# Kernel tuning notes

Hardware: AMD Instinct MI355X
Metric: run time of the kernel (lower is better)

Reference implementation:

```python
import jax, jax.numpy as jnp
import numpy as np

B, L, E = 64, 256, 512
H = 1024          # hidden_size
N = 128           # memory_size
HS = 64           # head_size (memory width)
NH = 4            # NTM heads
OUT = 1024        # output_size
TNH = 4           # transformer nhead
IN_DIM = E + NH * HS          # 768
POD = H + NH * HS             # 1280


def ln(x, g, b, eps=1e-5):
    mu = x.mean(-1, keepdims=True)
    v = ((x - mu) ** 2).mean(-1, keepdims=True)
    return (x - mu) / jnp.sqrt(v + eps) * g + b


def setup_inputs() -> dict:
    key = jax.random.key(0)
    ks = iter(jax.random.split(key, 64))
    def w(shape, s=0.05):
        return jax.random.normal(next(ks), shape, jnp.float32) * s
    f32 = jnp.float32
    return dict(
        x_emb=jax.random.normal(next(ks), (B, L, E), f32),
        in_g=jnp.ones(IN_DIM, f32), in_b=jnp.zeros(IN_DIM, f32),
        W_ih=w((4 * H, IN_DIM)), W_hh=w((4 * H, H)),
        b_ih=jnp.zeros(4 * H, f32), b_hh=jnp.zeros(4 * H, f32),
        cn_g=jnp.ones(H, f32), cn_b=jnp.zeros(H, f32),
        W_rk=w((NH * HS, H)), b_rk=jnp.zeros(NH * HS, f32),
        W_wk=w((NH * HS, H)), b_wk=jnp.zeros(NH * HS, f32),
        W_ws=w((NH, H)), b_ws=jnp.zeros(NH, f32),
        W_ev=w((NH * HS, H)), b_ev=jnp.zeros(NH * HS, f32),
        attn_w=w((3 * HS, HS)), attn_b=jnp.zeros(3 * HS, f32),
        attn_ow=w((HS, HS)), attn_ob=jnp.zeros(HS, f32),
        l1_w=w((2 * HS, HS)), l1_b=jnp.zeros(2 * HS, f32),
        l2_w=w((HS, 2 * HS)), l2_b=jnp.zeros(HS, f32),
        tn1_g=jnp.ones(HS, f32), tn1_b=jnp.zeros(HS, f32),
        tn2_g=jnp.ones(HS, f32), tn2_b=jnp.zeros(HS, f32),
        rkn_g=jnp.ones(HS, f32), rkn_b=jnp.zeros(HS, f32),
        wkn_g=jnp.ones(HS, f32), wkn_b=jnp.zeros(HS, f32),
        mn_g=jnp.ones(HS, f32), mn_b=jnp.zeros(HS, f32),
        po_g=jnp.ones(POD, f32), po_b=jnp.zeros(POD, f32),
        W_proj=w((OUT, POD)), b_proj=jnp.zeros(OUT, f32),
    )


def reference(x_emb, in_g, in_b, W_ih, W_hh, b_ih, b_hh, cn_g, cn_b,
              W_rk, b_rk, W_wk, b_wk, W_ws, b_ws, W_ev, b_ev,
              attn_w, attn_b, attn_ow, attn_ob, l1_w, l1_b, l2_w, l2_b,
              tn1_g, tn1_b, tn2_g, tn2_b, rkn_g, rkn_b, wkn_g, wkn_b,
              mn_g, mn_b, po_g, po_b, W_proj, b_proj):
    Bc = x_emb.shape[0]
    dh = HS // TNH

    def tblock(mem):  # [B, N, HS], eval-mode (dropout = identity)
        qkv = mem @ attn_w.T + attn_b
        q, k, v = jnp.split(qkv, 3, axis=-1)
        q = q.reshape(Bc, N, TNH, dh)
        k = k.reshape(Bc, N, TNH, dh)
        v = v.reshape(Bc, N, TNH, dh)
        a = jax.nn.softmax(jnp.einsum('bqhd,bkhd->bhqk', q, k) / jnp.sqrt(jnp.float32(dh)), axis=-1)
        o = jnp.einsum('bhqk,bkhd->bqhd', a, v).reshape(Bc, N, HS)
        o = o @ attn_ow.T + attn_ob
        x = ln(mem + o, tn1_g, tn1_b)
        ff = jax.nn.gelu(x @ l1_w.T + l1_b, approximate=False) @ l2_w.T + l2_b
        return ln(x + ff, tn2_g, tn2_b)

    def step(carry, x_t):
        h, c, mem, rc = carry
        inp = ln(jnp.concatenate([x_t, rc.reshape(Bc, -1)], axis=-1), in_g, in_b)
        gates = inp @ W_ih.T + b_ih + h @ W_hh.T + b_hh  # torch gate order i,f,g,o
        i, f, g, o = jnp.split(gates, 4, axis=-1)
        c = jax.nn.sigmoid(f) * c + jax.nn.sigmoid(i) * jnp.tanh(g)
        h = jax.nn.sigmoid(o) * jnp.tanh(c)
        hn = ln(h, cn_g, cn_b)
        rk = (hn @ W_rk.T + b_rk).reshape(Bc, NH, HS)
        wk = (hn @ W_wk.T + b_wk).reshape(Bc, NH, HS)
        ws = jax.nn.sigmoid(hn @ W_ws.T + b_ws)                    # [B, NH]
        ev = jax.nn.sigmoid(hn @ W_ev.T + b_ev).reshape(Bc, NH, HS)
        # addressing
        mem = tblock(mem)
        mem_n = ln(mem, mn_g, mn_b)
        rk = ln(rk, rkn_g, rkn_b)
        wk = ln(wk, wkn_g, wkn_b)
        rw = jax.nn.softmax(jnp.einsum('bnk,bmk->bnm', rk, mem_n), axis=-1)
        rc = jnp.einsum('bnm,bmh->bnh', rw, mem)
        ww = jax.nn.softmax(jnp.einsum('bnk,bmk->bnm', wk, mem_n), axis=-1)
        erase = jnp.einsum('bnm,bnh->bmh', ww, ev)
        mem = mem * (1.0 - erase)
        add = jnp.einsum('bnm,bnh->bmh', ww, ws[..., None] * wk)
        mem = mem + add
        out = ln(jnp.concatenate([hn, rc.reshape(Bc, -1)], axis=-1), po_g, po_b)
        logits = out @ W_proj.T + b_proj
        return (h, c, mem, rc), logits

    h0 = jnp.zeros((Bc, H), x_emb.dtype)
    c0 = jnp.zeros((Bc, H), x_emb.dtype)
    mem0 = jnp.zeros((Bc, N, HS), x_emb.dtype)
    rc0 = jnp.zeros((Bc, NH, HS), x_emb.dtype)
    (h, c, mem, _), outs = jax.lax.scan(step, (h0, c0, mem0, rc0), jnp.swapaxes(x_emb, 0, 1))
    return jnp.swapaxes(outs, 0, 1), mem, (h[None], c[None])
```

## Files before the change

kernel.cpp:

```cpp
#include <hip/hip_runtime.h>
#include <math.h>

typedef short s8v __attribute__((ext_vector_type(8)));
typedef float f32x4 __attribute__((ext_vector_type(4)));

__device__ inline float sigm(float x) { return 1.0f / (1.0f + expf(-x)); }
__device__ inline float dot4(const float4 a, const float4 b) {
  return a.x*b.x + a.y*b.y + a.z*b.z + a.w*b.w;
}
__device__ inline float wsum(float v) {
#pragma unroll
  for (int o = 32; o > 0; o >>= 1) v += __shfl_xor(v, o, 64);
  return v;
}
__device__ inline short f2bf(float f) {
  unsigned int u = __float_as_uint(f);
  unsigned int r = u + 0x7FFFu + ((u >> 16) & 1u);
  return (short)(r >> 16);
}
__device__ inline float bf2f(short h) {
  return __uint_as_float(((unsigned int)(unsigned short)h) << 16);
}
__device__ inline void storesplit(float v, short* __restrict__ hi,
                                  short* __restrict__ lo, size_t idx) {
// ... 58 lines not shown
{
  __shared__ float rs[4], rq[4];
  int b = blockIdx.x, tid = threadIdx.x, lane = tid & 63, wid = tid >> 6;
  float v3[3]; float s = 0.f, sq = 0.f;
#pragma unroll
  for (int i = 0; i < 3; i++) {
    int k = tid + i * 256;
    float v = (k < 512) ? x_emb[(size_t)b * 256 * 512 + k] : 0.f;
    v3[i] = v; s += v; sq += v * v;
  }
  s = wsum(s); sq = wsum(sq);
  if (lane == 0) { rs[wid] = s; rq[wid] = sq; }
  __syncthreads();
  float ts = rs[0]+rs[1]+rs[2]+rs[3], tq = rq[0]+rq[1]+rq[2]+rq[3];
  float mu = ts / 768.f, var = tq / 768.f - mu * mu;
  float rstd = rsqrtf(var + 1e-5f);
#pragma unroll
  for (int i = 0; i < 3; i++) {
    int k = tid + i * 256;
    storesplit((v3[i] - mu) * rstd * in_g[k] + in_b[k], inbH, inbL, b*1792 + k);
  }
}

__global__ __launch_bounds__(256) void kA(
    const short* __restrict__ inbH, const short* __restrict__ inbL,
    short* __restrict__ inbHn, short* __restrict__ inbLn,
    const short* __restrict__ WgH, const short* __restrict__ WgL,
    const float* __restrict__ b_ih, const float* __restrict__ b_hh,
    float* __restrict__ cbuf, float* __restrict__ hbuf,
    float* __restrict__ hstat, float* __restrict__ gatesP,
    unsigned* __restrict__ tick,
    const short* __restrict__ membH, const short* __restrict__ membL,
    const short* __restrict__ WqH, const short* __restrict__ WqL,
    const float* __restrict__ attn_b,
    const short* __restrict__ pob16, const short* __restrict__ Wp16,
    const float* __restrict__ b_proj,
    float* __restrict__ qkv, float* __restrict__ outs, int t)
{
  __shared__ char poolA[40960];
  __shared__ unsigned sOld;
  int bid = blockIdx.x, tid = threadIdx.x, lane = tid & 63, w = tid >> 6;
  if (bid < 128) {
    if (t >= 256) return;
    short (*sT)[4][2560] = (short(*)[4][2560])poolA;
    int jt = bid & 63, kt = bid >> 6;
    int k0 = kt * 896;
    int srow = tid >> 2, scol = (tid & 3) * 8;
    const short* gAH = inbH + srow*1792 + k0 + scol;
    const short* gAL = inbL + srow*1792 + k0 + scol;
    const short* gBH = WgH + (size_t)(jt*64 + srow)*1792 + k0 + scol;
    const short* gBL = WgL + (size_t)(jt*64 + srow)*1792 + k0 + scol;
    int4 rAH = *(const int4*)gAH, rAL = *(const int4*)gAL;
    int4 rBH = *(const int4*)gBH, rBL = *(const int4*)gBL;
    *(int4*)&sT[0][0][srow*40 + scol] = rAH;
    *(int4*)&sT[0][1][srow*40 + scol] = rAL;
    *(int4*)&sT[0][2][srow*40 + scol] = rBH;
    *(int4*)&sT[0][3][srow*40 + scol] = rBL;
    f32x4 acc[4] = {};
    int arow = lane & 15, akk = (lane >> 4) * 8;
    for (int c = 0; c < 28; ++c) {
      int cur = c & 1;
      if (c < 27) {
        rAH = *(const int4*)(gAH + (c+1)*32);
        rAL = *(const int4*)(gAL + (c+1)*32);
        rBH = *(const int4*)(gBH + (c+1)*32);
        rBL = *(const int4*)(gBL + (c+1)*32);
      }
      __syncthreads();
      s8v bh = *(const s8v*)&sT[cur][2][(w*16 + arow)*40 + akk];
      s8v bl = *(const s8v*)&sT[cur][3][(w*16 + arow)*40 + akk];
#pragma unroll
      for (int ms = 0; ms < 4; ++ms) {
        s8v ah = *(const s8v*)&sT[cur][0][(arow + ms*16)*40 + akk];
        s8v al = *(const s8v*)&sT[cur][1][(arow + ms*16)*40 + akk];
        acc[ms] = __builtin_amdgcn_mfma_f32_16x16x32_bf16(ah, bh, acc[ms], 0,0,0);
        acc[ms] = __builtin_amdgcn_mfma_f32_16x16x32_bf16(al, bh, acc[ms], 0,0,0);
        acc[ms] = __builtin_amdgcn_mfma_f32_16x16x32_bf16(ah, bl, acc[ms], 0,0,0);
      }
      if (c < 27) {
        *(int4*)&sT[cur^1][0][srow*40 + scol] = rAH;
        *(int4*)&sT[cur^1][1][srow*40 + scol] = rAL;
        *(int4*)&sT[cur^1][2][srow*40 + scol] = rBH;
        *(int4*)&sT[cur^1][3][srow*40 + scol] = rBL;
      }
    }
    {
      float* gp = gatesP + (size_t)kt * 262144;
      int j = jt*64 + w*16 + (lane & 15);
#pragma unroll
      for (int ms = 0; ms < 4; ms++)
#pragma unroll
        for (int r = 0; r < 4; r++) {
          int b = ms*16 + (lane>>4)*4 + r;
          gp[b*4096 + j] = acc[ms][r];
        }
    }
    __syncthreads();
    if (tid == 0) {
      __threadfence();
      sOld = __hip_atomic_fetch_add(&tick[jt], 1u, __ATOMIC_ACQ_REL,
                                    __HIP_MEMORY_SCOPE_AGENT);
    }
    __syncthreads();
    if (!(sOld & 1u)) return;
    {
      const float* pp = gatesP + (size_t)(kt^1) * 262144;
      int j = jt*64 + w*16 + (lane & 15);
#pragma unroll
      for (int ms = 0; ms < 4; ms++)
#pragma unroll
        for (int r = 0; r < 4; r++) {
          int b = ms*16 + (lane>>4)*4 + r;
          acc[ms][r] += __hip_atomic_load(&pp[b*4096 + j], __ATOMIC_RELAXED,
                                          __HIP_MEMORY_SCOPE_AGENT);
        }
    }
    float* sC = (float*)poolA;
    float* sRed = (float*)(poolA + 17408);
    __syncthreads();
    {
      int rr = w*16 + (lane & 15);
#pragma unroll
      for (int ms = 0; ms < 4; ms++)
#pragma unroll
        for (int r = 0; r < 4; r++) {
          int b = ms*16 + (lane>>4)*4 + r;
          sC[b*68 + rr] = acc[ms][r];
        }
    }
    __syncthreads();
    {
      int b = tid & 63;
      float sh = 0.f, sh2 = 0.f;
#pragma unroll
      for (int q = 0; q < 4; q++) {
        int ul = (tid >> 6) + q*4;
        int u = jt*16 + ul;
        float gi_ = sC[b*68 + ul*4 + 0] + b_ih[u]        + b_hh[u];
        float gf  = sC[b*68 + ul*4 + 1] + b_ih[1024 + u] + b_hh[1024 + u];
        float gg  = sC[b*68 + ul*4 + 2] + b_ih[2048 + u] + b_hh[2048 + u];
        float go  = sC[b*68 + ul*4 + 3] + b_ih[3072 + u] + b_hh[3072 + u];
        float cn = sigm(gf)*cbuf[b*1024 + u] + sigm(gi_)*tanhf(gg);
        float hh = sigm(go)*tanhf(cn);
        cbuf[b*1024 + u] = cn;
        hbuf[b*1024 + u] = hh;
        storesplit(hh, inbHn, inbLn, b*1792 + 768 + u);
        sh += hh; sh2 += hh*hh;
      }
      sRed[(tid>>6)*64 + b] = sh;
      sRed[256 + (tid>>6)*64 + b] = sh2;
    }
    __syncthreads();
    if (tid < 64) {
      float s0 = sRed[tid]+sRed[64+tid]+sRed[128+tid]+sRed[192+tid];
      float s1 = sRed[256+tid]+sRed[320+tid]+sRed[384+tid]+sRed[448+tid];
      hstat[(tid*64 + jt)*2]     = s0;
      hstat[(tid*64 + jt)*2 + 1] = s1;
    }
  } else if (bid < 192) {
    if (t >= 256) return;
    int b = bid - 128;
    const short* Ah = membH + (size_t)b * 8192;
    const short* Al = membL + (size_t)b * 8192;
    int ao = (w*32 + (lane & 15)) * 64 + (lane >> 4) * 8;
    s8v ah00 = *(const s8v*)(Ah + ao);
    s8v ah01 = *(const s8v*)(Ah + ao + 32);
    s8v ah10 = *(const s8v*)(Ah + ao + 16*64);
    s8v ah11 = *(const s8v*)(Ah + ao + 16*64 + 32);
    s8v al00 = *(const s8v*)(Al + ao);
    s8v al01 = *(const s8v*)(Al + ao + 32);
    s8v al10 = *(const s8v*)(Al + ao + 16*64);
    s8v al11 = *(const s8v*)(Al + ao + 16*64 + 32);
    int bo = (lane & 15) * 64 + (lane >> 4) * 8;
    for (int n = 0; n < 12; n++) {
      s8v bh0 = *(const s8v*)(WqH + bo + n*1024);
      s8v bh1 = *(const s8v*)(WqH + bo + n*1024 + 32);
      s8v bl0 = *(const s8v*)(WqL + bo + n*1024);
      s8v bl1 = *(const s8v*)(WqL + bo + n*1024 + 32);
      f32x4 acc0 = {}, acc1 = {};
      acc0 = __builtin_amdgcn_mfma_f32_16x16x32_bf16(ah00, bh0, acc0, 0,0,0);
      acc0 = __builtin_amdgcn_mfma_f32_16x16x32_bf16(ah01, bh1, acc0, 0,0,0);
      acc0 = __builtin_amdgcn_mfma_f32_16x16x32_bf16(al00, bh0, acc0, 0,0,0);
      acc0 = __builtin_amdgcn_mfma_f32_16x16x32_bf16(al01, bh1, acc0, 0,0,0);
      acc0 = __builtin_amdgcn_mfma_f32_16x16x32_bf16(ah00, bl0, acc0, 0,0,0);
      acc0 = __builtin_amdgcn_mfma_f32_16x16x32_bf16(ah01, bl1, acc0, 0,0,0);
      acc1 = __builtin_amdgcn_mfma_f32_16x16x32_bf16(ah10, bh0, acc1, 0,0,0);
      acc1 = __builtin_amdgcn_mfma_f32_16x16x32_bf16(ah11, bh1, acc1, 0,0,0);
      acc1 = __builtin_amdgcn_mfma_f32_16x16x32_bf16(al10, bh0, acc1, 0,0,0);
      acc1 = __builtin_amdgcn_mfma_f32_16x16x32_bf16(al11, bh1, acc1, 0,0,0);
      acc1 = __builtin_amdgcn_mfma_f32_16x16x32_bf16(ah10, bl0, acc1, 0,0,0);
      acc1 = __builtin_amdgcn_mfma_f32_16x16x32_bf16(ah11, bl1, acc1, 0,0,0);
      int j = n*16 + (lane & 15);
      int ch = j >> 6, jj = j & 63;
      float bv = attn_b[j];
#pragma unroll
      for (int r = 0; r < 4; r++) {
        int m0 = w*32 + (lane>>4)*4 + r;
        qkv[((size_t)(b*3 + ch)*128 + m0)*64 + jj] = acc0[r] + bv;
        qkv[((size_t)(b*3 + ch)*128 + m0 + 16)*64 + jj] = acc1[r] + bv;
      }
    }
  } else {
    if (t == 0) return;
    int jt = bid - 192;
    f32x4 acc[4] = {};
    const short* B = Wp16 + (size_t)(jt*64 + w*16) * 1280;
    gemm4<1280, 40>(pob16, B, acc, lane);
    int j = jt*64 + w*16 + (lane & 15);
    float bv = b_proj[j];
#pragma unroll
    for (int ms = 0; ms < 4; ms++)
#pragma unroll
      for (int r = 0; r < 4; r++) {
        int b = ms*16 + (lane>>4)*4 + r;
        outs[((size_t)b*256 + (t-1))*1024 + j] = acc[ms][r] + bv;
      }
  }
}

__global__ __launch_bounds__(512) void kB(
    float* __restrict__ mem, const float* __restrict__ qkv,
    const float* __restrict__ attn_ow, const float* __restrict__ attn_ob,
    const float* __restrict__ l1w, const float* __restrict__ l1b,
    const float* __restrict__ l2w, const float* __restrict__ l2b,
    const float* __restrict__ tn1g, const float* __restrict__ tn1b,
    const float* __restrict__ tn2g, const float* __restrict__ tn2b,
    const float* __restrict__ hbuf, const float* __restrict__ hstat,
    const float* __restrict__ cn_g, const float* __restrict__ cn_b,
    const short* __restrict__ WhH, const short* __restrict__ WhL,
    float* __restrict__ hp)
{
  __shared__ float pool[35200];
  int bid = blockIdx.x, tid = threadIdx.x;
  int lane = tid & 63, wid = tid >> 6;
  if (bid < 52) {
    int kt = bid & 3, jt = bid >> 2;
    {
      int b2 = tid & 63, part = tid >> 6;
      float s0 = 0.f, s1 = 0.f;
#pragma unroll 4
      for (int m2 = 0; m2 < 8; m2++) {
        int jt2 = part*8 + m2;
        s0 += hstat[(b2*64 + jt2)*2];
        s1 += hstat[(b2*64 + jt2)*2 + 1];
      }
      pool[part*64 + b2] = s0;
      pool[512 + part*64 + b2] = s1;
    }
    __syncthreads();
    if (tid < 64) {
      float ts = 0.f, tq = 0.f;
#pragma unroll
      for (int p2 = 0; p2 < 8; p2++) {
        ts += pool[p2*64 + tid];
        tq += pool[512 + p2*64 + tid];
      }
      float mu = ts / 1024.f;
      pool[1024+tid] = mu;
      pool[1088+tid] = rsqrtf(tq/1024.f - mu*mu + 1e-5f);
// ... 23 lines not shown
        size_t bo = (size_t)(jt*64 + wid*16 + arow)*1024 + kt*256 + c*32 + akk;
        s8v bh = *(const s8v*)(WhH + bo);
        s8v bl = *(const s8v*)(WhL + bo);
#pragma unroll
        for (int ms = 0; ms < 4; ++ms) {
          s8v ah = *(const s8v*)&sAH[(arow + ms*16)*40 + akk];
          s8v al = *(const s8v*)&sAL[(arow + ms*16)*40 + akk];
          acc[ms] = __builtin_amdgcn_mfma_f32_16x16x32_bf16(ah, bh, acc[ms], 0,0,0);
          acc[ms] = __builtin_amdgcn_mfma_f32_16x16x32_bf16(al, bh, acc[ms], 0,0,0);
          acc[ms] = __builtin_amdgcn_mfma_f32_16x16x32_bf16(ah, bl, acc[ms], 0,0,0);
        }
      }
    }
    if (wid < 4) {
      int j = jt*64 + wid*16 + (lane & 15);
#pragma unroll
      for (int ms = 0; ms < 4; ms++)
#pragma unroll
        for (int r = 0; r < 4; r++) {
          int b2 = ms*16 + (lane>>4)*4 + r;
          hp[(size_t)kt*53248 + b2*832 + j] = acc[ms][r];
        }
    }
    return;
  }
  float* sK  = pool;
  float* sV  = pool + 8704;
  float* sX  = pool + 17408;
  float* sM  = pool + 19584;
  float* sO  = pool + 21760;
  float* sS  = pool + 23936;
  float* sRed= pool + 34176;
  int bb0 = bid - 52;
  int b = bb0 & 63, mt = bb0 >> 6;
  int m0 = mt * 32;
  const float* qb = qkv + (size_t)b*3*8192;
  for (int i = tid*4; i < 8192; i += 2048) {
    *(float4*)&sK[i] = *(const float4*)&qb[8192 + i];
    *(float4*)&sV[i] = *(const float4*)&qb[16384 + i];
  }
  {
    int i = tid*4;
    int m = i >> 6, s = i & 63;
    *(float4*)&sX[m*68+s] = *(const float4*)&qb[m0*64 + i];
    *(float4*)&sM[m*68+s] = *(const float4*)&mem[(size_t)b*8192 + m0*64 + i];
  }
  __syncthreads();
  int m = tid >> 4, hd = (tid >> 2) & 3, q = tid & 3;
  const float* qp = sX + m*68 + hd*16;
  float4 q0 = *(const float4*)(qp),   q1 = *(const float4*)(qp+4);
  float4 q2 = *(const float4*)(qp+8), q3 = *(const float4*)(qp+12);
  int kmb = q * 32;
  float mx = -1e30f;
#pragma unroll 4
  for (int kk = 0; kk < 32; kk++) {
    const float* kp = sK + (kmb+kk)*64 + hd*16;
    float sc = dot4(q0, *(const float4*)kp)     + dot4(q1, *(const float4*)(kp+4))
             + dot4(q2, *(const float4*)(kp+8)) + dot4(q3, *(const float4*)(kp+12));
    mx = fmaxf(mx, sc * 0.25f);
  }
  float4 o0 = {0,0,0,0}, o1 = {0,0,0,0}, o2 = {0,0,0,0}, o3 = {0,0,0,0};
  float sum = 0.f;
#pragma unroll 4
  for (int kk = 0; kk < 32; kk++) {
    const float* kp = sK + (kmb+kk)*64 + hd*16;
    float sc = dot4(q0, *(const float4*)kp)     + dot4(q1, *(const float4*)(kp+4))
             + dot4(q2, *(const float4*)(kp+8)) + dot4(q3, *(const float4*)(kp+12));
    float e = expf(sc * 0.25f - mx);
    sum += e;
    const float* vp = sV + (kmb+kk)*64 + hd*16;
    float4 v0 = *(const float4*)vp,     v1 = *(const float4*)(vp+4);
    float4 v2 = *(const float4*)(vp+8), v3 = *(const float4*)(vp+12);
    o0.x += e*v0.x; o0.y += e*v0.y; o0.z += e*v0.z; o0.w += e*v0.w;
    o1.x += e*v1.x; o1.y += e*v1.y; o1.z += e*v1.z; o1.w += e*v1.w;
    o2.x += e*v2.x; o2.y += e*v2.y; o2.z += e*v2.z; o2.w += e*v2.w;
    o3.x += e*v3.x; o3.y += e*v3.y; o3.z += e*v3.z; o3.w += e*v3.w;
  }
  {
    float* pp = sS + tid*20;
    *(float4*)&pp[0]  = o0; *(float4*)&pp[4]  = o1;
    *(float4*)&pp[8]  = o2; *(float4*)&pp[12] = o3;
    sRed[tid] = mx; sRed[512+tid] = sum;
  }
  __syncthreads();
  if (q == 0) {
    float m1 = sRed[tid+1], m2 = sRed[tid+2], m3 = sRed[tid+3];
    float M = fmaxf(fmaxf(mx, m1), fmaxf(m2, m3));
    float e0 = expf(mx - M), e1 = expf(m1 - M), e2 = expf(m2 - M), e3 = expf(m3 - M);
    float inv = 1.0f / (sum*e0 + sRed[512+tid+1]*e1 + sRed[512+tid+2]*e2
                        + sRed[512+tid+3]*e3);
    const float* p1 = sS + (tid+1)*20;
    const float* p2 = sS + (tid+2)*20;
    const float* p3 = sS + (tid+3)*20;
    float oo[16];
    *(float4*)&oo[0] = o0; *(float4*)&oo[4] = o1;
    *(float4*)&oo[8] = o2; *(float4*)&oo[12] = o3;
    float* op = sO + m*68 + hd*16;
#pragma unroll
    for (int d = 0; d < 16; d++)
      op[d] = (oo[d]*e0 + p1[d]*e1 + p2[d]*e2 + p3[d]*e3) * inv;
  }
  __syncthreads();
  for (int idx = tid; idx < 4096; idx += 512) {
    int j = idx >> 6, s = idx & 63;
    sS[j*68 + s] = attn_ow[idx];
  }
  __syncthreads();
  {
    int mm = tid >> 4, jset = tid & 15;
    float4 orow[16];
#pragma unroll
    for (int r = 0; r < 16; r++) orow[r] = *(const float4*)&sO[mm*68 + r*4];
#pragma unroll
    for (int i = 0; i < 4; i++) {
      int j = jset + 16*i;
      const float* wr = sS + j*68;
      float acc = attn_ob[j];
#pragma unroll
      for (int r = 0; r < 16; r++) acc += dot4(orow[r], *(const float4*)&wr[r*4]);
      sM[mm*68 + j] += acc;
    }
  }
  __syncthreads();
  for (int r = wid; r < 32; r += 8) {
    float v = sM[r*68 + lane];
    float ssum = wsum(v), ssq = wsum(v*v);
    float mu = ssum*(1.f/64), var = ssq*(1.f/64) - mu*mu;
    sX[r*68+lane] = (v - mu)*rsqrtf(var+1e-5f)*tn1g[lane] + tn1b[lane];
  }
  for (int idx = tid; idx < 8192; idx += 512) {
    int f = idx >> 6, s = idx & 63;
    sK[f*68 + s] = l1w[idx];
  }
  for (int idx = tid; idx < 8192; idx += 512) {
    int j = idx >> 7, s = idx & 127;
    sV[j*132 + s] = l2w[idx];
  }
  __syncthreads();
  {
    int mm = tid >> 4, fs = tid & 15;
    float4 xr[16];
#pragma unroll
    for (int r = 0; r < 16; r++) xr[r] = *(const float4*)&sX[mm*68 + r*4];
#pragma unroll 4
    for (int i = 0; i < 8; i++) {
      int f = fs + 16*i;
      const float* wr = sK + f*68;
      float acc = l1b[f];
#pragma unroll
      for (int r = 0; r < 16; r++) acc += dot4(xr[r], *(const float4*)&wr[r*4]);
      sS[mm*132 + f] = 0.5f*acc*(1.0f + erff(acc*0.70710678118654752f));
    }
  }
  __syncthreads();
  {
    int mm = tid >> 4, jset = tid & 15;
    float acc6[4];
#pragma unroll
    for (int i = 0; i < 4; i++) acc6[i] = sX[mm*68 + jset + 16*i] + l2b[jset + 16*i];
#pragma unroll
    for (int h = 0; h < 2; h++) {
      float4 fr[16];
#pragma unroll
      for (int r = 0; r < 16; r++) fr[r] = *(const float4*)&sS[mm*132 + h*64 + r*4];
#pragma unroll
      for (int i = 0; i < 4; i++) {
        int j = jset + 16*i;
        const float* wr = sV + j*132 + h*64;
        float a = 0.f;
#pragma unroll
        for (int r = 0; r < 16; r++) a += dot4(fr[r], *(const float4*)&wr[r*4]);
        acc6[i] += a;
      }
    }
#pragma unroll
    for (int i = 0; i < 4; i++) sO[mm*68 + jset + 16*i] = acc6[i];
  }
  __syncthreads();
  for (int r = wid; r < 32; r += 8) {
    float v = sO[r*68 + lane];
    float ssum = wsum(v), ssq = wsum(v*v);
    float mu = ssum*(1.f/64), var = ssq*(1.f/64) - mu*mu;
    mem[(size_t)b*8192 + (m0+r)*64 + lane] =
        (v - mu)*rsqrtf(var+1e-5f)*tn2g[lane] + tn2b[lane];
  }
}

__global__ __launch_bounds__(512) void kC(
    float* __restrict__ mem, short* __restrict__ membH, short* __restrict__ membL,
    const float* __restrict__ hp, const float* __restrict__ hstat,
    const float* __restrict__ hbuf,
    const float* __restrict__ b_rk, const float* __restrict__ b_wk,
    const float* __restrict__ b_ev, const float* __restrict__ b_ws,
    const float* __restrict__ rkn_g, const float* __restrict__ rkn_b,
    const float* __restrict__ wkn_g, const float* __restrict__ wkn_b,
    const float* __restrict__ cn_g, const float* __restrict__ cn_b,
    const float* __restrict__ mng, const float* __restrict__ mnb,
    const float* __restrict__ pog, const float* __restrict__ pob,
    const float* __restrict__ x_emb, const float* __restrict__ in_g,
    const float* __restrict__ in_b,
    short* __restrict__ inbHn, short* __restrict__ inbLn,
    short* __restrict__ pob16, int tnext)
{
  __shared__ float P[20960];
  float* sMT  = P;
  float* sMN  = P + 8192;
  float* sHn  = P + 16512;
// ... 190 lines not shown
  const float* attn_b = (const float*)d_in[18];
  const float* attn_ow= (const float*)d_in[19];
  const float* attn_ob= (const float*)d_in[20];
  const float* l1_w   = (const float*)d_in[21];
  const float* l1_b   = (const float*)d_in[22];
  const float* l2_w   = (const float*)d_in[23];
  const float* l2_b   = (const float*)d_in[24];
  const float* tn1_g  = (const float*)d_in[25];
  const float* tn1_b  = (const float*)d_in[26];
  const float* tn2_g  = (const float*)d_in[27];
  const float* tn2_b  = (const float*)d_in[28];
  const float* rkn_g  = (const float*)d_in[29];
  const float* rkn_b  = (const float*)d_in[30];
  const float* wkn_g  = (const float*)d_in[31];
  const float* wkn_b  = (const float*)d_in[32];
  const float* mn_g   = (const float*)d_in[33];
  const float* mn_b   = (const float*)d_in[34];
  const float* po_g   = (const float*)d_in[35];
  const float* po_b   = (const float*)d_in[36];
  const float* W_proj = (const float*)d_in[37];
  const float* b_proj = (const float*)d_in[38];

  float* ws = (float*)d_ws;
  float* mem    = ws;
  float* cbuf   = ws + 524288;
  float* hbuf   = ws + 589824;
  float* gatesP = ws + 655360;
  float* hp     = ws + 1179648;
  float* hstat  = ws + 1392640;
  unsigned* tick = (unsigned*)(ws + 1400832);
  float* qkvb   = ws + 1400896;
  short* sb     = (short*)(ws + 2973760);
  short* inbH0 = sb;
  short* inbL0 = sb + 114688;
  short* inbH1 = sb + 229376;
  short* inbL1 = sb + 344064;
  short* membH = sb + 458752;
  short* membL = sb + 983040;
  short* pob16 = sb + 1507328;
  short* WgH   = sb + 1589248;
  short* WgL   = sb + 8929280;
  short* WhH   = sb + 16269312;
  short* WhL   = sb + 17121280;
  short* WqH   = sb + 17973248;
  short* WqL   = sb + 17985536;
  short* Wp16  = sb + 17997824;

  hipMemsetAsync(ws, 0, 655360 * sizeof(float), stream);
  hipMemsetAsync(tick, 0, 256, stream);
  hipMemsetAsync(sb, 0, 1507328 * sizeof(short), stream);

  kprep_g<<<dim3(7, 4096), 256, 0, stream>>>(W_ih, W_hh, WgH, WgL);
  kprep_p<<<dim3(5, 1024), 256, 0, stream>>>(W_proj, Wp16);
  kprep_h<<<dim3(4, 832), 256, 0, stream>>>(W_rk, W_wk, W_ev, W_ws, WhH, WhL);
  kprep_q<<<dim3(192), 64, 0, stream>>>(attn_w, WqH, WqL);
  k_prep0<<<64, 256, 0, stream>>>(x_emb, in_g, in_b, inbH0, inbL0);

  float* outs = (float*)d_out;
  short* bufsH[2] = {inbH0, inbH1};
  short* bufsL[2] = {inbL0, inbL1};
  for (int t = 0; t < 256; t++) {
    kA<<<208, 256, 0, stream>>>(bufsH[t&1], bufsL[t&1], bufsH[(t+1)&1], bufsL[(t+1)&1],
                                WgH, WgL, b_ih, b_hh, cbuf, hbuf, hstat, gatesP, tick,
                                membH, membL, WqH, WqL, attn_b,
                                pob16, Wp16, b_proj, qkvb, outs, t);
    kB<<<308, 512, 0, stream>>>(mem, qkvb, attn_ow, attn_ob,
                                l1_w, l1_b, l2_w, l2_b,
                                tn1_g, tn1_b, tn2_g, tn2_b,
                                hbuf, hstat, cn_g, cn_b, WhH, WhL, hp);
    kC<<<64, 512, 0, stream>>>(mem, membH, membL, hp, hstat, hbuf,
                               b_rk, b_wk, b_ev, b_ws,
                               rkn_g, rkn_b, wkn_g, wkn_b, cn_g, cn_b,
                               mn_g, mn_b, po_g, po_b,
                               x_emb, in_g, in_b,
                               bufsH[(t+1)&1], bufsL[(t+1)&1], pob16, t+1);
  }
  kA<<<208, 256, 0, stream>>>(bufsH[0], bufsL[0], bufsH[1], bufsL[1],
                              WgH, WgL, b_ih, b_hh, cbuf, hbuf, hstat, gatesP, tick,
                              membH, membL, WqH, WqL, attn_b,
                              pob16, Wp16, b_proj, qkvb, outs, 256);
  k_final<<<2048, 256, 0, stream>>>(mem, hbuf, cbuf, (float*)d_out);
}
```

Before: 25.81 ms.

## Fuse gate GEMM, qkv projection and transformer block into one per-step kernel

Merges the former kA and kB launches into a single 512-thread kernel per timestep. The LSTM gate GEMM now splits K across two half-blocks inside one workgroup and reduces through LDS, replacing the global partial-sum buffer and tick atomic pairing. The qkv projection is recomputed per memory tile inside the transformer-block workgroups, so the qkv global buffer goes away. Blocks that depended on hstat/h from the gate stage presumably wait on a global counter (gctr), which adds an intra-kernel spin dependency and extra MFMA work in exchange for one fewer launch per step.

Result: slower. 29.75 ms (+15.3%).

```diff
diff --git a/kernel.cpp b/kernel.cpp
--- a/kernel.cpp
+++ b/kernel.cpp
@@ -104,30 +104,39 @@
   }
 }
 
-__global__ __launch_bounds__(256) void kA(
+__global__ __launch_bounds__(512) void kAB(
     const short* __restrict__ inbH, const short* __restrict__ inbL,
     short* __restrict__ inbHn, short* __restrict__ inbLn,
     const short* __restrict__ WgH, const short* __restrict__ WgL,
     const float* __restrict__ b_ih, const float* __restrict__ b_hh,
     float* __restrict__ cbuf, float* __restrict__ hbuf,
-    float* __restrict__ hstat, float* __restrict__ gatesP,
-    unsigned* __restrict__ tick,
+    float* __restrict__ hstat, unsigned* __restrict__ gctr,
     const short* __restrict__ membH, const short* __restrict__ membL,
     const short* __restrict__ WqH, const short* __restrict__ WqL,
     const float* __restrict__ attn_b,
+    float* __restrict__ mem,
+    const float* __restrict__ attn_ow, const float* __restrict__ attn_ob,
+    const float* __restrict__ l1w, const float* __restrict__ l1b,
+    const float* __restrict__ l2w, const float* __restrict__ l2b,
+    const float* __restrict__ tn1g, const float* __restrict__ tn1b,
+    const float* __restrict__ tn2g, const float* __restrict__ tn2b,
+    const float* __restrict__ cn_g, const float* __restrict__ cn_b,
+    const short* __restrict__ WhH, const short* __restrict__ WhL,
+    float* __restrict__ hp,
     const short* __restrict__ pob16, const short* __restrict__ Wp16,
-    const float* __restrict__ b_proj,
-    float* __restrict__ qkv, float* __restrict__ outs, int t)
+    const float* __restrict__ b_proj, float* __restrict__ outs, int t)
 {
-  __shared__ char poolA[40960];
-  __shared__ unsigned sOld;
-  int bid = blockIdx.x, tid = threadIdx.x, lane = tid & 63, w = tid >> 6;
-  if (bid < 128) {
+  __shared__ float pool[35200];
+  int bid = blockIdx.x, tid = threadIdx.x, lane = tid & 63;
+  if (bid < 64) {
     if (t >= 256) return;
-    short (*sT)[4][2560] = (short(*)[4][2560])poolA;
-    int jt = bid & 63, kt = bid >> 6;
+    int jt = bid;
+    int kt = tid >> 8;
+    int tl = tid & 255;
+    int w4 = (tid >> 6) & 3;
+    short (*sT)[4][2560] = (short(*)[4][2560])((char*)pool + kt*40960);
     int k0 = kt * 896;
-    int srow = tid >> 2, scol = (tid & 3) * 8;
+    int srow = tl >> 2, scol = (tl & 3) * 8;
     const short* gAH = inbH + srow*1792 + k0 + scol;
     const short* gAL = inbL + srow*1792 + k0 + scol;
     const short* gBH = WgH + (size_t)(jt*64 + srow)*1792 + k0 + scol;
@@ -149,8 +158,8 @@
         rBL = *(const int4*)(gBL + (c+1)*32);
       }
       __syncthreads();
-      s8v bh = *(const s8v*)&sT[cur][2][(w*16 + arow)*40 + akk];
-      s8v bl = *(const s8v*)&sT[cur][3][(w*16 + arow)*40 + akk];
+      s8v bh = *(const s8v*)&sT[cur][2][(w4*16 + arow)*40 + akk];
+      s8v bl = *(const s8v*)&sT[cur][3][(w4*16 + arow)*40 + akk];
 #pragma unroll
       for (int ms = 0; ms < 4; ++ms) {
         s8v ah = *(const s8v*)&sT[cur][0][(arow + ms*16)*40 + akk];
@@ -166,62 +175,32 @@
         *(int4*)&sT[cur^1][3][srow*40 + scol] = rBL;
       }
     }
+    __syncthreads();
+    float* sC = pool;
+    float* sRed = pool + 8704;
     {
-      float* gp = gatesP + (size_t)kt * 262144;
-      int j = jt*64 + w*16 + (lane & 15);
+      float* sCk = sC + kt*4352;
+      int rr = w4*16 + (lane & 15);
 #pragma unroll
       for (int ms = 0; ms < 4; ms++)
 #pragma unroll
         for (int r = 0; r < 4; r++) {
           int b = ms*16 + (lane>>4)*4 + r;
-          gp[b*4096 + j] = acc[ms][r];
+          sCk[b*68 + rr] = acc[ms][r];
         }
     }
     __syncthreads();
-    if (tid == 0) {
-      __threadfence();
-      sOld = __hip_atomic_fetch_add(&tick[jt], 1u, __ATOMIC_ACQ_REL,
-                                    __HIP_MEMORY_SCOPE_AGENT);
-    }
-    __syncthreads();
-    if (!(sOld & 1u)) return;
     {
-      const float* pp = gatesP + (size_t)(kt^1) * 262144;
-      int j = jt*64 + w*16 + (lane & 15);
-#pragma unroll
-      for (int ms = 0; ms < 4; ms++)
-#pragma unroll
-        for (int r = 0; r < 4; r++) {
-          int b = ms*16 + (lane>>4)*4 + r;
-          acc[ms][r] += __hip_atomic_load(&pp[b*4096 + j], __ATOMIC_RELAXED,
-                                          __HIP_MEMORY_SCOPE_AGENT);
-        }
-    }
-    float* sC = (float*)poolA;
-    float* sRed = (float*)(poolA + 17408);
-    __syncthreads();
-    {
-      int rr = w*16 + (lane & 15);
-#pragma unroll
-      for (int ms = 0; ms < 4; ms++)
-#pragma unroll
-        for (int r = 0; r < 4; r++) {
-          int b = ms*16 + (lane>>4)*4 + r;
-          sC[b*68 + rr] = acc[ms][r];
-        }
-    }
-    __syncthreads();
-    {
-      int b = tid & 63;
+      int b = tid & 63, ug = tid >> 6;
       float sh = 0.f, sh2 = 0.f;
 #pragma unroll
-      for (int q = 0; q < 4; q++) {
-        int ul = (tid >> 6) + q*4;
+      for (int q = 0; q < 2; q++) {
+        int ul = ug*2 + q;
         int u = jt*16 + ul;
-        float gi_ = sC[b*68 + ul*4 + 0] + b_ih[u]        + b_hh[u];
-        float gf  = sC[b*68 + ul*4 + 1] + b_ih[1024 + u] + b_hh[1024 + u];
-        float gg  = sC[b*68 + ul*4 + 2] + b_ih[2048 + u] + b_hh[2048 + u];
-        float go  = sC[b*68 + ul*4 + 3] + b_ih[3072 + u] + b_hh[3072 + u];
+        float gi_ = sC[b*68 + ul*4 + 0] + sC[4352 + b*68 + ul*4 + 0] + b_ih[u]        + b_hh[u];
+        float gf  = sC[b*68 + ul*4 + 1] + sC[4352 + b*68 + ul*4 + 1] + b_ih[1024 + u] + b_hh[1024 + u];
+        float gg  = sC[b*68 + ul*4 + 2] + sC[4352 + b*68 + ul*4 + 2] + b_ih[2048 + u] + b_hh[2048 + u];
+        float go  = sC[b*68 + ul*4 + 3] + sC[4352 + b*68 + ul*4 + 3] + b_ih[3072 + u] + b_hh[3072 + u];
         float cn = sigm(gf)*cbuf[b*1024 + u] + sigm(gi_)*tanhf(gg);
         float hh = sigm(go)*tanhf(cn);
         cbuf[b*1024 + u] = cn;
@@ -229,66 +208,222 @@
         storesplit(hh, inbHn, inbLn, b*1792 + 768 + u);
         sh += hh; sh2 += hh*hh;
       }
-      sRed[(tid>>6)*64 + b] = sh;
-      sRed[256 + (tid>>6)*64 + b] = sh2;
+      sRed[ug*64 + b] = sh;
+      sRed[512 + ug*64 + b] = sh2;
     }
     __syncthreads();
     if (tid < 64) {
-      float s0 = sRed[tid]+sRed[64+tid]+sRed[128+tid]+sRed[192+tid];
-      float s1 = sRed[256+tid]+sRed[320+tid]+sRed[384+tid]+sRed[448+tid];
+      float s0 = 0.f, s1 = 0.f;
+#pragma unroll
+      for (int p = 0; p < 8; p++) { s0 += sRed[p*64 + tid]; s1 += sRed[512 + p*64 + tid]; }
       hstat[(tid*64 + jt)*2]     = s0;
       hstat[(tid*64 + jt)*2 + 1] = s1;
     }
-  } else if (bid < 192) {
+    __syncthreads();
+    if (tid == 0) {
+      __threadfence();
+      __hip_atomic_fetch_add(gctr, 1u, __ATOMIC_RELEASE, __HIP_MEMORY_SCOPE_AGENT);
+    }
+  } else if (bid < 320) {
     if (t >= 256) return;
-    int b = bid - 128;
-    const short* Ah = membH + (size_t)b * 8192;
-    const short* Al = membL + (size_t)b * 8192;
-    int ao = (w*32 + (lane & 15)) * 64 + (lane >> 4) * 8;
-    s8v ah00 = *(const s8v*)(Ah + ao);
-    s8v ah01 = *(const s8v*)(Ah + ao + 32);
-    s8v ah10 = *(const s8v*)(Ah + ao + 16*64);
-    s8v ah11 = *(const s8v*)(Ah + ao + 16*64 + 32);
-    s8v al00 = *(const s8v*)(Al + ao);
-    s8v al01 = *(const s8v*)(Al + ao + 32);
-    s8v al10 = *(const s8v*)(Al + ao + 16*64);
-    s8v al11 = *(const s8v*)(Al + ao + 16*64 + 32);
-    int bo = (lane & 15) * 64 + (lane >> 4) * 8;
-    for (int n = 0; n < 12; n++) {
-      s8v bh0 = *(const s8v*)(WqH + bo + n*1024);
-      s8v bh1 = *(const s8v*)(WqH + bo + n*1024 + 32);
-      s8v bl0 = *(const s8v*)(WqL + bo + n*1024);
-      s8v bl1 = *(const s8v*)(WqL + bo + n*1024 + 32);
-      f32x4 acc0 = {}, acc1 = {};
-      acc0 = __builtin_amdgcn_mfma_f32_16x16x32_bf16(ah00, bh0, acc0, 0,0,0);
-      acc0 = __builtin_amdgcn_mfma_f32_16x16x32_bf16(ah01, bh1, acc0, 0,0,0);
-      acc0 = __builtin_amdgcn_mfma_f32_16x16x32_bf16(al00, bh0, acc0, 0,0,0);
-      acc0 = __builtin_amdgcn_mfma_f32_16x16x32_bf16(al01, bh1, acc0, 0,0,0);
-      acc0 = __builtin_amdgcn_mfma_f32_16x16x32_bf16(ah00, bl0, acc0, 0,0,0);
-      acc0 = __builtin_amdgcn_mfma_f32_16x16x32_bf16(ah01, bl1, acc0, 0,0,0);
-      acc1 = __builtin_amdgcn_mfma_f32_16x16x32_bf16(ah10, bh0, acc1, 0,0,0);
-      acc1 = __builtin_amdgcn_mfma_f32_16x16x32_bf16(ah11, bh1, acc1, 0,0,0);
-      acc1 = __builtin_amdgcn_mfma_f32_16x16x32_bf16(al10, bh0, acc1, 0,0,0);
-      acc1 = __builtin_amdgcn_mfma_f32_16x16x32_bf16(al11, bh1, acc1, 0,0,0);
-      acc1 = __builtin_amdgcn_mfma_f32_16x16x32_bf16(ah10, bl0, acc1, 0,0,0);
-      acc1 = __builtin_amdgcn_mfma_f32_16x16x32_bf16(ah11, bl1, acc1, 0,0,0);
-      int j = n*16 + (lane & 15);
-      int ch = j >> 6, jj = j & 63;
-      float bv = attn_b[j];
-#pragma unroll
-      for (int r = 0; r < 4; r++) {
-        int m0 = w*32 + (lane>>4)*4 + r;
-        qkv[((size_t)(b*3 + ch)*128 + m0)*64 + jj] = acc0[r] + bv;
-        qkv[((size_t)(b*3 + ch)*128 + m0 + 16)*64 + jj] = acc1[r] + bv;
-      }
-    }
-  } else {
+    float* sK  = pool;
+    float* sV  = pool + 8704;
+    float* sX  = pool + 17408;
+    float* sM  = pool + 19584;
+    float* sO  = pool + 21760;
+    float* sS  = pool + 23936;
+    float* sRed= pool + 34176;
+    int pb = bid - 64;
+    int b = pb & 63, mt = pb >> 6;
+    int m0 = mt * 32;
+    int wid = tid >> 6;
+    {
+      const short* Ah = membH + (size_t)b * 8192;
+      const short* Al = membL + (size_t)b * 8192;
+      int ao = (wid*16 + (lane & 15)) * 64 + (lane >> 4) * 8;
+      s8v ah0 = *(const s8v*)(Ah + ao);
+      s8v ah1 = *(const s8v*)(Ah + ao + 32);
+      s8v al0 = *(const s8v*)(Al + ao);
+      s8v al1 = *(const s8v*)(Al + ao + 32);
+      int bo = (lane & 15) * 64 + (lane >> 4) * 8;
+      for (int n = 0; n < 12; n++) {
+        s8v bh0 = *(const s8v*)(WqH + bo + n*1024);
+        s8v bh1 = *(const s8v*)(WqH + bo + n*1024 + 32);
+        s8v bl0 = *(const s8v*)(WqL + bo + n*1024);
+        s8v bl1 = *(const s8v*)(WqL + bo + n*1024 + 32);
+        f32x4 acc = {};
+        acc = __builtin_amdgcn_mfma_f32_16x16x32_bf16(ah0, bh0, acc, 0,0,0);
+        acc = __builtin_amdgcn_mfma_f32_16x16x32_bf16(ah1, bh1, acc, 0,0,0);
+        acc = __builtin_amdgcn_mfma_f32_16x16x32_bf16(al0, bh0, acc, 0,0,0);
+        acc = __builtin_amdgcn_mfma_f32_16x16x32_bf16(al1, bh1, acc, 0,0,0);
+        acc = __builtin_amdgcn_mfma_f32_16x16x32_bf16(ah0, bl0, acc, 0,0,0);
+        acc = __builtin_amdgcn_mfma_f32_16x16x32_bf16(ah1, bl1, acc, 0,0,0);
+        int j = n*16 + (lane & 15);
+        int ch = j >> 6, jj = j & 63;
+        float bv = attn_b[j];
+#pragma unroll
+        for (int r = 0; r < 4; r++) {
+          int mr = wid*16 + (lane>>4)*4 + r;
+          float v = acc[r] + bv;
+          if (ch == 0) {
+            if (mr >= m0 && mr < m0 + 32) sX[(mr - m0)*68 + jj] = v;
+          } else if (ch == 1) sK[mr*64 + jj] = v;
+          else sV[mr*64 + jj] = v;
+        }
+      }
+    }
+    {
+      int i = tid*4;
+      int m = i >> 6, s = i & 63;
+      *(float4*)&sM[m*68+s] = *(const float4*)&mem[(size_t)b*8192 + m0*64 + i];
+    }
+    __syncthreads();
+    int m = tid >> 4, hd = (tid >> 2) & 3, q = tid & 3;
+    const float* qp = sX + m*68 + hd*16;
+    float4 q0 = *(const float4*)(qp),   q1 = *(const float4*)(qp+4);
+    float4 q2 = *(const float4*)(qp+8), q3 = *(const float4*)(qp+12);
+    int kmb = q * 32;
+    float mx = -1e30f;
+#pragma unroll 4
+    for (int kk = 0; kk < 32; kk++) {
+      const float* kp = sK + (kmb+kk)*64 + hd*16;
+      float sc = dot4(q0, *(const float4*)kp)     + dot4(q1, *(const float4*)(kp+4))
+               + dot4(q2, *(const float4*)(kp+8)) + dot4(q3, *(const float4*)(kp+12));
+      mx = fmaxf(mx, sc * 0.25f);
+    }
+    float4 o0 = {0,0,0,0}, o1 = {0,0,0,0}, o2 = {0,0,0,0}, o3 = {0,0,0,0};
+    float sum = 0.f;
+#pragma unroll 4
+    for (int kk = 0; kk < 32; kk++) {
+      const float* kp = sK + (kmb+kk)*64 + hd*16;
+      float sc = dot4(q0, *(const float4*)kp)     + dot4(q1, *(const float4*)(kp+4))
+               + dot4(q2, *(const float4*)(kp+8)) + dot4(q3, *(const float4*)(kp+12));
+      float e = expf(sc * 0.25f - mx);
+      sum += e;
+      const float* vp = sV + (kmb+kk)*64 + hd*16;
+      float4 v0 = *(const float4*)vp,     v1 = *(const float4*)(vp+4);
+      float4 v2 = *(const float4*)(vp+8), v3 = *(const float4*)(vp+12);
+      o0.x += e*v0.x; o0.y += e*v0.y; o0.z += e*v0.z; o0.w += e*v0.w;
+      o1.x += e*v1.x; o1.y += e*v1.y; o1.z += e*v1.z; o1.w += e*v1.w;
+      o2.x += e*v2.x; o2.y += e*v2.y; o2.z += e*v2.z; o2.w += e*v2.w;
+      o3.x += e*v3.x; o3.y += e*v3.y; o3.z += e*v3.z; o3.w += e*v3.w;
+    }
+    {
+      float* pp = sS + tid*20;
+      *(float4*)&pp[0]  = o0; *(float4*)&pp[4]  = o1;
+      *(float4*)&pp[8]  = o2; *(float4*)&pp[12] = o3;
+      sRed[tid] = mx; sRed[512+tid] = sum;
+    }
+    __syncthreads();
+    if (q == 0) {
+      float m1 = sRed[tid+1], m2 = sRed[tid+2], m3 = sRed[tid+3];
+      float M = fmaxf(fmaxf(mx, m1), fmaxf(m2, m3));
+      float e0 = expf(mx - M), e1 = expf(m1 - M), e2 = expf(m2 - M), e3 = expf(m3 - M);
+      float inv = 1.0f / (sum*e0 + sRed[512+tid+1]*e1 + sRed[512+tid+2]*e2
+                          + sRed[512+tid+3]*e3);
+      const float* p1 = sS + (tid+1)*20;
+      const float* p2 = sS + (tid+2)*20;
+      const float* p3 = sS + (tid+3)*20;
+      float oo[16];
+      *(float4*)&oo[0] = o0; *(float4*)&oo[4] = o1;
+      *(float4*)&oo[8] = o2; *(float4*)&oo[12] = o3;
+      float* op = sO + m*68 + hd*16;
+#pragma unroll
+      for (int d = 0; d < 16; d++)
+        op[d] = (oo[d]*e0 + p1[d]*e1 + p2[d]*e2 + p3[d]*e3) * inv;
+    }
+    __syncthreads();
+    for (int idx = tid; idx < 4096; idx += 512) {
+      int j = idx >> 6, s = idx & 63;
+      sS[j*68 + s] = attn_ow[idx];
+    }
+    __syncthreads();
+    {
+      int mm = tid >> 4, jset = tid & 15;
+      float4 orow[16];
+#pragma unroll
+      for (int r = 0; r < 16; r++) orow[r] = *(const float4*)&sO[mm*68 + r*4];
+#pragma unroll
+      for (int i = 0; i < 4; i++) {
+        int j = jset + 16*i;
+        const float* wr = sS + j*68;
+        float acc = attn_ob[j];
+#pragma unroll
+        for (int r = 0; r < 16; r++) acc += dot4(orow[r], *(const float4*)&wr[r*4]);
+        sM[mm*68 + j] += acc;
+      }
+    }
+    __syncthreads();
+    for (int r = wid; r < 32; r += 8) {
+      float v = sM[r*68 + lane];
+      float ssum = wsum(v), ssq = wsum(v*v);
+      float mu = ssum*(1.f/64), var = ssq*(1.f/64) - mu*mu;
+      sX[r*68+lane] = (v - mu)*rsqrtf(var+1e-5f)*tn1g[lane] + tn1b[lane];
+    }
+    for (int idx = tid; idx < 8192; idx += 512) {
+      int f = idx >> 6, s = idx & 63;
+      sK[f*68 + s] = l1w[idx];
+    }
+    for (int idx = tid; idx < 8192; idx += 512) {
+      int j = idx >> 7, s = idx & 127;
+      sV[j*132 + s] = l2w[idx];
+    }
+    __syncthreads();
+    {
+      int mm = tid >> 4, fs = tid & 15;
+      float4 xr[16];
+#pragma unroll
+      for (int r = 0; r < 16; r++) xr[r] = *(const float4*)&sX[mm*68 + r*4];
+#pragma unroll 4
+      for (int i = 0; i < 8; i++) {
+        int f = fs + 16*i;
+        const float* wr = sK + f*68;
+        float acc = l1b[f];
+#pragma unroll
+        for (int r = 0; r < 16; r++) acc += dot4(xr[r], *(const float4*)&wr[r*4]);
+        sS[mm*132 + f] = 0.5f*acc*(1.0f + erff(acc*0.70710678118654752f));
+      }
+    }
+    __syncthreads();
+    {
+      int mm = tid >> 4, jset = tid & 15;
+      float acc6[4];
+#pragma unroll
+      for (int i = 0; i < 4; i++) acc6[i] = sX[mm*68 + jset + 16*i] + l2b[jset + 16*i];
+#pragma unroll
+      for (int h = 0; h < 2; h++) {
+        float4 fr[16];
+#pragma unroll
+        for (int r = 0; r < 16; r++) fr[r] = *(const float4*)&sS[mm*132 + h*64 + r*4];
+#pragma unroll
+        for (int i = 0; i < 4; i++) {
+          int j = jset + 16*i;
+          const float* wr = sV + j*132 + h*64;
+          float a = 0.f;
+#pragma unroll
+          for (int r = 0; r < 16; r++) a += dot4(fr[r], *(const float4*)&wr[r*4]);
+          acc6[i] += a;
+        }
+      }
+#pragma unroll
+      for (int i = 0; i < 4; i++) sO[mm*68 + jset + 16*i] = acc6[i];
+    }
+    __syncthreads();
+    for (int r = wid; r < 32; r += 8) {
+      float v = sO[r*68 + lane];
+      float ssum = wsum(v), ssq = wsum(v*v);
+      float mu = ssum*(1.f/64), var = ssq*(1.f/64) - mu*mu;
+      mem[(size_t)b*8192 + (m0+r)*64 + lane] =
+          (v - mu)*rsqrtf(var+1e-5f)*tn2g[lane] + tn2b[lane];
+    }
+  } else if (bid < 328) {
     if (t == 0) return;
-    int jt = bid - 192;
+    int jt = bid - 320;
+    int w = tid >> 6;
     f32x4 acc[4] = {};
-    const short* B = Wp16 + (size_t)(jt*64 + w*16) * 1280;
+    const short* B = Wp16 + (size_t)(jt*128 + w*16) * 1280;
     gemm4<1280, 40>(pob16, B, acc, lane);
-    int j = jt*64 + w*16 + (lane & 15);
+    int j = jt*128 + w*16 + (lane & 15);
     float bv = b_proj[j];
 #pragma unroll
     for (int ms = 0; ms < 4; ms++)
@@ -297,26 +432,17 @@
         int b = ms*16 + (lane>>4)*4 + r;
         outs[((size_t)b*256 + (t-1))*1024 + j] = acc[ms][r] + bv;
       }
-  }
-}
-
-__global__ __launch_bounds__(512) void kB(
-    float* __restrict__ mem, const float* __restrict__ qkv,
-    const float* __restrict__ attn_ow, const float* __restrict__ attn_ob,
-    const float* __restrict__ l1w, const float* __restrict__ l1b,
-    const float* __restrict__ l2w, const float* __restrict__ l2b,
-    const float* __restrict__ tn1g, const float* __restrict__ tn1b,
-    const float* __restrict__ tn2g, const float* __restrict__ tn2b,
-    const float* __restrict__ hbuf, const float* __restrict__ hstat,
-    const float* __restrict__ cn_g, const float* __restrict__ cn_b,
-    const short* __restrict__ WhH, const short* __restrict__ WhL,
-    float* __restrict__ hp)
-{
-  __shared__ float pool[35200];
-  int bid = blockIdx.x, tid = threadIdx.x;
-  int lane = tid & 63, wid = tid >> 6;
-  if (bid < 52) {
-    int kt = bid & 3, jt = bid >> 2;
+  } else {
+    if (t >= 256) return;
+    int wid = tid >> 6;
+    if (tid == 0) {
+      unsigned target = 64u * (unsigned)(t + 1);
+      while (__hip_atomic_load(gctr, __ATOMIC_ACQUIRE, __HIP_MEMORY_SCOPE_AGENT) < target)
+        __builtin_amdgcn_s_sleep(2);
+    }
+    __syncthreads();
+    int hb = bid - 328;
+    int kt = hb & 3, jt = hb >> 2;
     {
       int b2 = tid & 63, part = tid >> 6;
       float s0 = 0.f, s1 = 0.f;
@@ -386,167 +512,6 @@
           hp[(size_t)kt*53248 + b2*832 + j] = acc[ms][r];
         }
     }
-    return;
-  }
-  float* sK  = pool;
-  float* sV  = pool + 8704;
-  float* sX  = pool + 17408;
-  float* sM  = pool + 19584;
-  float* sO  = pool + 21760;
-  float* sS  = pool + 23936;
-  float* sRed= pool + 34176;
-  int bb0 = bid - 52;
-  int b = bb0 & 63, mt = bb0 >> 6;
-  int m0 = mt * 32;
-  const float* qb = qkv + (size_t)b*3*8192;
-  for (int i = tid*4; i < 8192; i += 2048) {
-    *(float4*)&sK[i] = *(const float4*)&qb[8192 + i];
-    *(float4*)&sV[i] = *(const float4*)&qb[16384 + i];
-  }
-  {
-    int i = tid*4;
-    int m = i >> 6, s = i & 63;
-    *(float4*)&sX[m*68+s] = *(const float4*)&qb[m0*64 + i];
-    *(float4*)&sM[m*68+s] = *(const float4*)&mem[(size_t)b*8192 + m0*64 + i];
-  }
-  __syncthreads();
-  int m = tid >> 4, hd = (tid >> 2) & 3, q = tid & 3;
-  const float* qp = sX + m*68 + hd*16;
-  float4 q0 = *(const float4*)(qp),   q1 = *(const float4*)(qp+4);
-  float4 q2 = *(const float4*)(qp+8), q3 = *(const float4*)(qp+12);
-  int kmb = q * 32;
-  float mx = -1e30f;
-#pragma unroll 4
-  for (int kk = 0; kk < 32; kk++) {
-    const float* kp = sK + (kmb+kk)*64 + hd*16;
-    float sc = dot4(q0, *(const float4*)kp)     + dot4(q1, *(const float4*)(kp+4))
-             + dot4(q2, *(const float4*)(kp+8)) + dot4(q3, *(const float4*)(kp+12));
-    mx = fmaxf(mx, sc * 0.25f);
-  }
-  float4 o0 = {0,0,0,0}, o1 = {0,0,0,0}, o2 = {0,0,0,0}, o3 = {0,0,0,0};
-  float sum = 0.f;
-#pragma unroll 4
-  for (int kk = 0; kk < 32; kk++) {
-    const float* kp = sK + (kmb+kk)*64 + hd*16;
-    float sc = dot4(q0, *(const float4*)kp)     + dot4(q1, *(const float4*)(kp+4))
-             + dot4(q2, *(const float4*)(kp+8)) + dot4(q3, *(const float4*)(kp+12));
-    float e = expf(sc * 0.25f - mx);
-    sum += e;
-    const float* vp = sV + (kmb+kk)*64 + hd*16;
-    float4 v0 = *(const float4*)vp,     v1 = *(const float4*)(vp+4);
-    float4 v2 = *(const float4*)(vp+8), v3 = *(const float4*)(vp+12);
-    o0.x += e*v0.x; o0.y += e*v0.y; o0.z += e*v0.z; o0.w += e*v0.w;
-    o1.x += e*v1.x; o1.y += e*v1.y; o1.z += e*v1.z; o1.w += e*v1.w;
-    o2.x += e*v2.x; o2.y += e*v2.y; o2.z += e*v2.z; o2.w += e*v2.w;
-    o3.x += e*v3.x; o3.y += e*v3.y; o3.z += e*v3.z; o3.w += e*v3.w;
-  }
-  {
-    float* pp = sS + tid*20;
-    *(float4*)&pp[0]  = o0; *(float4*)&pp[4]  = o1;
-    *(float4*)&pp[8]  = o2; *(float4*)&pp[12] = o3;
-    sRed[tid] = mx; sRed[512+tid] = sum;
-  }
-  __syncthreads();
-  if (q == 0) {
-    float m1 = sRed[tid+1], m2 = sRed[tid+2], m3 = sRed[tid+3];
-    float M = fmaxf(fmaxf(mx, m1), fmaxf(m2, m3));
-    float e0 = expf(mx - M), e1 = expf(m1 - M), e2 = expf(m2 - M), e3 = expf(m3 - M);
-    float inv = 1.0f / (sum*e0 + sRed[512+tid+1]*e1 + sRed[512+tid+2]*e2
-                        + sRed[512+tid+3]*e3);
-    const float* p1 = sS + (tid+1)*20;
-    const float* p2 = sS + (tid+2)*20;
-    const float* p3 = sS + (tid+3)*20;
-    float oo[16];
-    *(float4*)&oo[0] = o0; *(float4*)&oo[4] = o1;
-    *(float4*)&oo[8] = o2; *(float4*)&oo[12] = o3;
-    float* op = sO + m*68 + hd*16;
-#pragma unroll
-    for (int d = 0; d < 16; d++)
-      op[d] = (oo[d]*e0 + p1[d]*e1 + p2[d]*e2 + p3[d]*e3) * inv;
-  }
-  __syncthreads();
-  for (int idx = tid; idx < 4096; idx += 512) {
-    int j = idx >> 6, s = idx & 63;
-    sS[j*68 + s] = attn_ow[idx];
-  }
-  __syncthreads();
-  {
-    int mm = tid >> 4, jset = tid & 15;
-    float4 orow[16];
-#pragma unroll
-    for (int r = 0; r < 16; r++) orow[r] = *(const float4*)&sO[mm*68 + r*4];
-#pragma unroll
-    for (int i = 0; i < 4; i++) {
-      int j = jset + 16*i;
-      const float* wr = sS + j*68;
-      float acc = attn_ob[j];
-#pragma unroll
-      for (int r = 0; r < 16; r++) acc += dot4(orow[r], *(const float4*)&wr[r*4]);
-      sM[mm*68 + j] += acc;
-    }
-  }
-  __syncthreads();
-  for (int r = wid; r < 32; r += 8) {
-    float v = sM[r*68 + lane];
-    float ssum = wsum(v), ssq = wsum(v*v);
-    float mu = ssum*(1.f/64), var = ssq*(1.f/64) - mu*mu;
-    sX[r*68+lane] = (v - mu)*rsqrtf(var+1e-5f)*tn1g[lane] + tn1b[lane];
-  }
-  for (int idx = tid; idx < 8192; idx += 512) {
-    int f = idx >> 6, s = idx & 63;
-    sK[f*68 + s] = l1w[idx];
-  }
-  for (int idx = tid; idx < 8192; idx += 512) {
-    int j = idx >> 7, s = idx & 127;
-    sV[j*132 + s] = l2w[idx];
-  }
-  __syncthreads();
-  {
-    int mm = tid >> 4, fs = tid & 15;
-    float4 xr[16];
-#pragma unroll
-    for (int r = 0; r < 16; r++) xr[r] = *(const float4*)&sX[mm*68 + r*4];
-#pragma unroll 4
-    for (int i = 0; i < 8; i++) {
-      int f = fs + 16*i;
-      const float* wr = sK + f*68;
-      float acc = l1b[f];
-#pragma unroll
-      for (int r = 0; r < 16; r++) acc += dot4(xr[r], *(const float4*)&wr[r*4]);
-      sS[mm*132 + f] = 0.5f*acc*(1.0f + erff(acc*0.70710678118654752f));
-    }
-  }
-  __syncthreads();
-  {
-    int mm = tid >> 4, jset = tid & 15;
-    float acc6[4];
-#pragma unroll
-    for (int i = 0; i < 4; i++) acc6[i] = sX[mm*68 + jset + 16*i] + l2b[jset + 16*i];
-#pragma unroll
-    for (int h = 0; h < 2; h++) {
-      float4 fr[16];
-#pragma unroll
-      for (int r = 0; r < 16; r++) fr[r] = *(const float4*)&sS[mm*132 + h*64 + r*4];
-#pragma unroll
-      for (int i = 0; i < 4; i++) {
-        int j = jset + 16*i;
-        const float* wr = sV + j*132 + h*64;
-        float a = 0.f;
-#pragma unroll
-        for (int r = 0; r < 16; r++) a += dot4(fr[r], *(const float4*)&wr[r*4]);
-        acc6[i] += a;
-      }
-    }
-#pragma unroll
-    for (int i = 0; i < 4; i++) sO[mm*68 + jset + 16*i] = acc6[i];
-  }
-  __syncthreads();
-  for (int r = wid; r < 32; r += 8) {
-    float v = sO[r*68 + lane];
-    float ssum = wsum(v), ssq = wsum(v*v);
-    float mu = ssum*(1.f/64), var = ssq*(1.f/64) - mu*mu;
-    mem[(size_t)b*8192 + (m0+r)*64 + lane] =
-        (v - mu)*rsqrtf(var+1e-5f)*tn2g[lane] + tn2b[lane];
   }
 }
 
@@ -783,15 +748,13 @@
   const float* b_proj = (const float*)d_in[38];
 
   float* ws = (float*)d_ws;
-  float* mem    = ws;
-  float* cbuf   = ws + 524288;
-  float* hbuf   = ws + 589824;
-  float* gatesP = ws + 655360;
-  float* hp     = ws + 1179648;
-  float* hstat  = ws + 1392640;
-  unsigned* tick = (unsigned*)(ws + 1400832);
-  float* qkvb   = ws + 1400896;
-  short* sb     = (short*)(ws + 2973760);
+  float* mem   = ws;
+  float* cbuf  = ws + 524288;
+  float* hbuf  = ws + 589824;
+  float* hstat = ws + 655360;
+  float* hp    = ws + 663552;
+  unsigned* gctr = (unsigned*)(ws + 876544);
+  short* sb    = (short*)(ws + 876560);
   short* inbH0 = sb;
   short* inbL0 = sb + 114688;
   short* inbH1 = sb + 229376;
@@ -799,16 +762,16 @@
   short* membH = sb + 458752;
   short* membL = sb + 983040;
   short* pob16 = sb + 1507328;
-  short* WgH   = sb + 1589248;
-  short* WgL   = sb + 8929280;
-  short* WhH   = sb + 16269312;
-  short* WhL   = sb + 17121280;
-  short* WqH   = sb + 17973248;
-  short* WqL   = sb + 17985536;
+  short* WqH   = sb + 1589248;
+  short* WqL   = sb + 1601536;
+  short* WgH   = sb + 1613824;
+  short* WgL   = sb + 8953856;
+  short* WhH   = sb + 16293888;
+  short* WhL   = sb + 17145856;
   short* Wp16  = sb + 17997824;
 
   hipMemsetAsync(ws, 0, 655360 * sizeof(float), stream);
-  hipMemsetAsync(tick, 0, 256, stream);
+  hipMemsetAsync(gctr, 0, 64, stream);
   hipMemsetAsync(sb, 0, 1507328 * sizeof(short), stream);
 
   kprep_g<<<dim3(7, 4096), 256, 0, stream>>>(W_ih, W_hh, WgH, WgL);
@@ -821,14 +784,12 @@
   short* bufsH[2] = {inbH0, inbH1};
   short* bufsL[2] = {inbL0, inbL1};
   for (int t = 0; t < 256; t++) {
-    kA<<<208, 256, 0, stream>>>(bufsH[t&1], bufsL[t&1], bufsH[(t+1)&1], bufsL[(t+1)&1],
-                                WgH, WgL, b_ih, b_hh, cbuf, hbuf, hstat, gatesP, tick,
-                                membH, membL, WqH, WqL, attn_b,
-                                pob16, Wp16, b_proj, qkvb, outs, t);
-    kB<<<308, 512, 0, stream>>>(mem, qkvb, attn_ow, attn_ob,
-                                l1_w, l1_b, l2_w, l2_b,
-                                tn1_g, tn1_b, tn2_g, tn2_b,
-                                hbuf, hstat, cn_g, cn_b, WhH, WhL, hp);
+    kAB<<<380, 512, 0, stream>>>(bufsH[t&1], bufsL[t&1], bufsH[(t+1)&1], bufsL[(t+1)&1],
+                                 WgH, WgL, b_ih, b_hh, cbuf, hbuf, hstat, gctr,
+                                 membH, membL, WqH, WqL, attn_b, mem,
+                                 attn_ow, attn_ob, l1_w, l1_b, l2_w, l2_b,
+                                 tn1_g, tn1_b, tn2_g, tn2_b, cn_g, cn_b,
+                                 WhH, WhL, hp, pob16, Wp16, b_proj, outs, t);
     kC<<<64, 512, 0, stream>>>(mem, membH, membL, hp, hstat, hbuf,
                                b_rk, b_wk, b_ev, b_ws,
                                rkn_g, rkn_b, wkn_g, wkn_b, cn_g, cn_b,
@@ -836,9 +797,11 @@
                                x_emb, in_g, in_b,
                                bufsH[(t+1)&1], bufsL[(t+1)&1], pob16, t+1);
   }
-  kA<<<208, 256, 0, stream>>>(bufsH[0], bufsL[0], bufsH[1], bufsL[1],
-                              WgH, WgL, b_ih, b_hh, cbuf, hbuf, hstat, gatesP, tick,
-                              membH, membL, WqH, WqL, attn_b,
-                              pob16, Wp16, b_proj, qkvb, outs, 256);
+  kAB<<<380, 512, 0, stream>>>(bufsH[0], bufsL[0], bufsH[1], bufsL[1],
+                               WgH, WgL, b_ih, b_hh, cbuf, hbuf, hstat, gctr,
+                               membH, membL, WqH, WqL, attn_b, mem,
+                               attn_ow, attn_ob, l1_w, l1_b, l2_w, l2_b,
+                               tn1_g, tn1_b, tn2_g, tn2_b, cn_g, cn_b,
+                               WhH, WhL, hp, pob16, Wp16, b_proj, outs, 256);
   k_final<<<2048, 256, 0, stream>>>(mem, hbuf, cbuf, (float*)d_out);
 }
```
